# Performance work log

Hardware: AMD Instinct MI355X
Metric: run time of the kernel (lower is better)

The kernel has to match this reference:

```python
import jax, jax.numpy as jnp
import numpy as np

N_NODES = 100000

def setup_inputs() -> dict:
    key = jax.random.key(0)
    k1, k2, k3 = jax.random.split(key, 3)
    x = jax.random.normal(k1, (N_NODES, 128), dtype=jnp.float32)
    edge_index = jax.random.randint(k2, (2, 1600000), 0, N_NODES, dtype=jnp.int64)
    W = jax.random.normal(k3, (128, 128), dtype=jnp.float32) * 0.05  # Linear weight [out, in]
    b = jnp.zeros((128,), dtype=jnp.float32)
    return {"x": x, "edge_index": edge_index, "W": W, "b": b}

def reference(x, edge_index, W, b):
    # GCNConv (PyG defaults): normalize=True, add_self_loops=True, bias=True.
    N = x.shape[0]
    # 1) linear transform (no bias inside)
    h = x @ W.T  # [N, H]
    # 2) add self loops
    loops = jnp.arange(N, dtype=edge_index.dtype)
    src = jnp.concatenate([edge_index[0], loops])  # source (x_j)
    dst = jnp.concatenate([edge_index[1], loops])  # target (aggregation)
    # 3) symmetric degree normalization: deg over target nodes with unit weights
    deg = jax.ops.segment_sum(jnp.ones_like(dst, dtype=h.dtype), dst, num_segments=N)
    dinv = jnp.where(deg > 0, jax.lax.rsqrt(deg), 0.0)
    norm = dinv[src] * dinv[dst]  # [E+N]
    # 4) gather-scale-scatter aggregation
    msgs = h[src] * norm[:, None]  # [E+N, H]
    out = jax.ops.segment_sum(msgs, dst, num_segments=N)
    # 5) bias
    return out + b
```

## Files before the change

### kernel.cpp

```cpp
#include <hip/hip_runtime.h>

#define H 128
#define NREG 8
#define KE 16
#define TILE (256 * KE)
#define LINB 512
#define B2T 2048
#define SCAP 3072
#define RCAP 220160

typedef __attribute__((ext_vector_type(8))) short short8_t;
typedef __attribute__((ext_vector_type(4))) float float4_t;

__device__ __forceinline__ ushort f2bf(float f) {
  uint u = __float_as_uint(f);
  u += 0x7fff + ((u >> 16) & 1);
  return (ushort)(u >> 16);
}
__device__ __forceinline__ float bflo(uint v) { return __uint_as_float(v << 16); }
__device__ __forceinline__ float bfhi(uint v) { return __uint_as_float(v & 0xffff0000u); }

__global__ __launch_bounds__(256) void k_linbin(const float* __restrict__ x, const float* __restrict__ W,
                                                ushort* __restrict__ hs,
                                                const int* __restrict__ src, const int* __restrict__ dst,
                                                int* gcur, int* __restrict__ breg,
                                                int N, int E, int npr) {
  __shared__ int cntw[4][NREG];
  __shared__ int basew[4][NREG];
  __shared__ int lpre8[NREG + 1];
  __shared__ int gbase8[NREG];
  __shared__ int staged[TILE];
  const int tid = threadIdx.x;

  if (blockIdx.x < LINB) {
    const int lane = tid & 63;
    const int wid  = tid >> 6;
    const int rg   = wid >> 1;
    const int cg   = wid & 1;
    const int q    = lane >> 4;
    const int lm   = lane & 15;

    short8_t bfr[4][4];
    #pragma unroll
    for (int kk = 0; kk < 4; ++kk) {
      #pragma unroll
      for (int nf = 0; nf < 4; ++nf) {
        const float* wp = W + (cg * 64 + nf * 16 + lm) * 128 + kk * 32 + q * 8;
        float4_t w0 = *(const float4_t*)wp;
        float4_t w1 = *(const float4_t*)(wp + 4);
        union { short8_t s; ushort u[8]; } t;
        t.u[0] = f2bf(w0.x); t.u[1] = f2bf(w0.y); t.u[2] = f2bf(w0.z); t.u[3] = f2bf(w0.w);
        t.u[4] = f2bf(w1.x); t.u[5] = f2bf(w1.y); t.u[6] = f2bf(w1.z); t.u[7] = f2bf(w1.w);
        bfr[kk][nf] = t.s;
      }
    }

    const int ntiles = (N + 31) / 32;
    for (int tile = blockIdx.x; tile < ntiles; tile += LINB) {
      const int n0 = tile * 32;
      const int arow = n0 + rg * 16 + lm;
      const int arow_c = (arow < N) ? arow : (N - 1);
      const float* xp = x + (long)arow_c * H + q * 8;
      short8_t afr[4];
      #pragma unroll
      for (int kk = 0; kk < 4; ++kk) {
        float4_t x0 = *(const float4_t*)(xp + kk * 32);
        float4_t x1 = *(const float4_t*)(xp + kk * 32 + 4);
        union { short8_t s; ushort u[8]; } t;
        t.u[0] = f2bf(x0.x); t.u[1] = f2bf(x0.y); t.u[2] = f2bf(x0.z); t.u[3] = f2bf(x0.w);
        t.u[4] = f2bf(x1.x); t.u[5] = f2bf(x1.y); t.u[6] = f2bf(x1.z); t.u[7] = f2bf(x1.w);
        afr[kk] = t.s;
      }

      float4_t acc[4];
      #pragma unroll
      for (int nf = 0; nf < 4; ++nf) acc[nf] = (float4_t){0.f, 0.f, 0.f, 0.f};
      #pragma unroll
      for (int kk = 0; kk < 4; ++kk) {
        #pragma unroll
        for (int nf = 0; nf < 4; ++nf)
          acc[nf] = __builtin_amdgcn_mfma_f32_16x16x32_bf16(bfr[kk][nf], afr[kk], acc[nf], 0, 0, 0);
      }

      if (arow < N) {
        ushort* hrow = hs + (size_t)arow * H + cg * 64 + q * 4;
        #pragma unroll
        for (int nf = 0; nf < 4; ++nf) {
          uint2 o;
          o.x = (uint)f2bf(acc[nf][0]) | ((uint)f2bf(acc[nf][1]) << 16);
          o.y = (uint)f2bf(acc[nf][2]) | ((uint)f2bf(acc[nf][3]) << 16);
          *(uint2*)(hrow + nf * 16) = o;
        }
      }
    }
  } else {
    const int bb = blockIdx.x - LINB;
    const int wv = tid >> 6;
    if (tid < 32) cntw[tid >> 3][tid & 7] = 0;
    __syncthreads();
    const int base = bb * TILE;
    int pk[KE], r[KE], off[KE];
    #pragma unroll
    for (int k = 0; k < KE; ++k) {
      const int e = base + k * 256 + tid;
      if (e < E) {
        const int s = src[e], d = dst[e];
        r[k] = (int)((unsigned)d / (unsigned)npr);
        pk[k] = (s << 14) | (d - r[k] * npr);
        off[k] = atomicAdd(&cntw[wv][r[k]], 1);
      } else r[k] = -1;
    }
    __syncthreads();
    if (tid == 0) {
      int acc = 0;
      #pragma unroll
      for (int j = 0; j < NREG; ++j) {
        lpre8[j] = acc;
        #pragma unroll
        for (int w2 = 0; w2 < 4; ++w2) { basew[w2][j] = acc; acc += cntw[w2][j]; }
      }
      lpre8[NREG] = acc;
    }
    __syncthreads();
    if (tid < NREG) gbase8[tid] = atomicAdd(&gcur[tid], lpre8[tid + 1] - lpre8[tid]);
    #pragma unroll
    for (int k = 0; k < KE; ++k)
      if (r[k] >= 0) staged[basew[wv][r[k]] + off[k]] = pk[k];
    __syncthreads();
    const int tot = lpre8[NREG];
    for (int i = tid; i < tot; i += 256) {
      int reg = 0;
      #pragma unroll
      for (int j = 1; j < NREG; ++j) reg += (i >= lpre8[j]);
      const int p = gbase8[reg] + (i - lpre8[reg]);
      if (p < RCAP) breg[reg * RCAP + p] = staged[i];
    }
  }
}

__global__ __launch_bounds__(256) void k_bin2(const int* __restrict__ breg, const int* __restrict__ gcur,
                                              int* cur2, int* __restrict__ bsub, int nsub) {
  __shared__ int cnt[128], lcur[128], lpre[128], gb[128];
  __shared__ int staged[B2T];
  const int tid = threadIdx.x;
  const int r = blockIdx.x & 7;
  const int t0 = (blockIdx.x >> 3) * B2T;
  const int total = min(gcur[r], RCAP);
  if (t0 >= total) return;
  const int cntT = min(B2T, total - t0);
  for (int i = tid; i < 128; i += 256) { cnt[i] = 0; lcur[i] = 0; }
  __syncthreads();
  const int* bp = breg + (size_t)r * RCAP + t0;
  for (int i = tid; i < cntT; i += 256) atomicAdd(&cnt[(bp[i] >> 7) & 127], 1);
  __syncthreads();
  if (tid < 128) lpre[tid] = cnt[tid];
  __syncthreads();
  for (int off = 1; off < 128; off <<= 1) {
    int v = 0;
    if (tid < 128 && tid >= off) v = lpre[tid - off];
    __syncthreads();
    if (tid < 128) lpre[tid] += v;
    __syncthreads();
  }
  if (tid < 128) {
    lpre[tid] -= cnt[tid];
    const int c = cnt[tid];
    gb[tid] = c ? atomicAdd(&cur2[r * nsub + tid], c) : 0;
  }
  __syncthreads();
  for (int i = tid; i < cntT; i += 256) {
    const int v = bp[i];
    const int sub = (v >> 7) & 127;
    const int pos = lpre[sub] + atomicAdd(&lcur[sub], 1);
    staged[pos] = (sub << 24) | ((v >> 14) << 7) | (v & 127);
  }
  __syncthreads();
  for (int i = tid; i < cntT; i += 256) {
    const int v = staged[i];
    const int sub = (int)((unsigned)v >> 24);
    const int pos = gb[sub] + (i - lpre[sub]);
    if (pos < SCAP) bsub[((size_t)(r * nsub + sub)) * SCAP + pos] = v & 0xFFFFFF;
  }
}

__global__ __launch_bounds__(256) void k_fill3(const int* __restrict__ bsub, const int* __restrict__ cur2,
                                               float* __restrict__ dinv, uint4* __restrict__ rowinfo,
                                               int* __restrict__ csr, int N, int npr, int nsub) {
  __shared__ int cnt[128], pre[128], lcur[128];
  __shared__ int stage[SCAP], sorted[SCAP];
  const int tid = threadIdx.x;
  const int r = blockIdx.x & 7;
  const int sub = blockIdx.x >> 3;
  const int sid = r * nsub + sub;
  const int gn0 = r * npr + sub * 128;
  int nodes = npr - sub * 128; if (nodes > 128) nodes = 128;
  if (N - gn0 < nodes) nodes = N - gn0;
  if (nodes <= 0) return;
  if (tid < 128) cnt[tid] = 0;
  __syncthreads();

  const int slotbase = sid * SCAP;
  const int cc = min(cur2[sid], SCAP);
  const int* bp = bsub + (size_t)slotbase;
  for (int i = tid; i < cc; i += 256) {
    const int v = bp[i];
    stage[i] = v;
    atomicAdd(&cnt[v & 127], 1);
  }
  __syncthreads();

  if (tid < 128) pre[tid] = cnt[tid];
  __syncthreads();
  for (int off = 1; off < 128; off <<= 1) {
    int v = 0;
    if (tid < 128 && tid >= off) v = pre[tid - off];
    __syncthreads();
    if (tid < 128) pre[tid] += v;
    __syncthreads();
  }
  if (tid < 128) pre[tid] -= cnt[tid];
  __syncthreads();

  if (tid < nodes) {
    const int c = cnt[tid];
    const float dv = rsqrtf((float)(1 + c));
    dinv[gn0 + tid] = dv;
    rowinfo[gn0 + tid] = make_uint4((uint)(slotbase + pre[tid]), (uint)c, __float_as_uint(dv), 0u);
    lcur[tid] = pre[tid];
  }
  __syncthreads();

  for (int i = tid; i < cc; i += 256) {
    const int v = stage[i];
    const int p = atomicAdd(&lcur[v & 127], 1);
    sorted[p] = (int)((unsigned)v >> 7);
  }
  __syncthreads();
  for (int i = tid; i < cc; i += 256) csr[slotbase + i] = sorted[i];
}

#define ACCS(q, ds) { a0 = fmaf(bflo((q).x), ds, a0); a1 = fmaf(bfhi((q).x), ds, a1); \
                      a2 = fmaf(bflo((q).y), ds, a2); a3 = fmaf(bfhi((q).y), ds, a3); \
                      a4 = fmaf(bflo((q).z), ds, a4); a5 = fmaf(bfhi((q).z), ds, a5); \
                      a6 = fmaf(bflo((q).w), ds, a6); a7 = fmaf(bfhi((q).w), ds, a7); }
__global__ __launch_bounds__(256) void k_agg(const ushort* __restrict__ hs, const float* __restrict__ dinv,
                                             const uint4* __restrict__ rowinfo, const int* __restrict__ csr,
                                             const float* __restrict__ bias, float* __restrict__ out,
                                             int N, int npr) {
  const int r = blockIdx.x & 7;
  const int ln = (blockIdx.x >> 3) * 16 + (threadIdx.x >> 4);
  if (ln >= npr) return;
  const int d = r * npr + ln;
  if (d >= N) return;
  const int j = threadIdx.x & 15;
  const uint4* hp = (const uint4*)hs;

  const uint4 info = rowinfo[d];
  int i = (int)info.x;
  int cnt = (int)info.y;
  const float dd = __uint_as_float(info.z);

  const uint4 qs = hp[(size_t)d * 16 + j];
  float a0 = bflo(qs.x) * dd, a1 = bfhi(qs.x) * dd, a2 = bflo(qs.y) * dd, a3 = bfhi(qs.y) * dd;
  float a4 = bflo(qs.z) * dd, a5 = bfhi(qs.z) * dd, a6 = bflo(qs.w) * dd, a7 = bfhi(qs.w) * dd;

  for (; cnt >= 8; cnt -= 8, i += 8) {
    const int s0 = csr[i],     s1 = csr[i + 1], s2 = csr[i + 2], s3 = csr[i + 3];
    const int s4 = csr[i + 4], s5 = csr[i + 5], s6 = csr[i + 6], s7 = csr[i + 7];
    const float d0 = dinv[s0], d1 = dinv[s1], d2 = dinv[s2], d3 = dinv[s3];
    const float d4 = dinv[s4], d5 = dinv[s5], d6 = dinv[s6], d7 = dinv[s7];
    const uint4 qA = hp[(size_t)s0 * 16 + j];
    const uint4 qB = hp[(size_t)s1 * 16 + j];
    const uint4 qC = hp[(size_t)s2 * 16 + j];
    const uint4 qD = hp[(size_t)s3 * 16 + j];
    const uint4 qE = hp[(size_t)s4 * 16 + j];
    const uint4 qF = hp[(size_t)s5 * 16 + j];
    const uint4 qG = hp[(size_t)s6 * 16 + j];
    const uint4 qH = hp[(size_t)s7 * 16 + j];
    ACCS(qA, d0) ACCS(qB, d1) ACCS(qC, d2) ACCS(qD, d3)
    ACCS(qE, d4) ACCS(qF, d5) ACCS(qG, d6) ACCS(qH, d7)
  }
  if (cnt >= 4) {
    const int s0 = csr[i], s1 = csr[i + 1], s2 = csr[i + 2], s3 = csr[i + 3];
    const float d0 = dinv[s0], d1 = dinv[s1], d2 = dinv[s2], d3 = dinv[s3];
    const uint4 qA = hp[(size_t)s0 * 16 + j];
    const uint4 qB = hp[(size_t)s1 * 16 + j];
    const uint4 qC = hp[(size_t)s2 * 16 + j];
    const uint4 qD = hp[(size_t)s3 * 16 + j];
    ACCS(qA, d0) ACCS(qB, d1) ACCS(qC, d2) ACCS(qD, d3)
    cnt -= 4; i += 4;
  }
  for (; cnt > 0; --cnt, ++i) {
    const int s = csr[i];
    const float ds = dinv[s];
    const uint4 q = hp[(size_t)s * 16 + j];
    ACCS(q, ds)
  }

  const float4_t b0 = *(const float4_t*)(bias + j * 8);
  const float4_t b1 = *(const float4_t*)(bias + j * 8 + 4);
  float4_t o0, o1;
  o0.x = a0 * dd + b0.x; o0.y = a1 * dd + b0.y; o0.z = a2 * dd + b0.z; o0.w = a3 * dd + b0.w;
  o1.x = a4 * dd + b1.x; o1.y = a5 * dd + b1.y; o1.z = a6 * dd + b1.z; o1.w = a7 * dd + b1.w;
  __builtin_nontemporal_store(o0, (float4_t*)(out + (size_t)d * H + j * 8));
  __builtin_nontemporal_store(o1, (float4_t*)(out + (size_t)d * H + j * 8 + 4));
}

extern "C" void kernel_launch(void* const* d_in, const int* in_sizes, int n_in,
                              void* d_out, int out_size, void* d_ws, size_t ws_size,
                              hipStream_t stream) {
  const float* x = (const float*)d_in[0];
  const int*   edge = (const int*)d_in[1];
  const float* W = (const float*)d_in[2];
  const float* b = (const float*)d_in[3];
  float* out = (float*)d_out;

  const int N = in_sizes[0] / H;
  const int E = in_sizes[1] / 2;
  const int* src = edge;
  const int* dst = edge + E;
  const int npr  = (N + NREG - 1) / NREG;
  const int nsub = (npr + 127) / 128;
  const int nsubt = NREG * nsub;

  char* w = (char*)d_ws;
  ushort* hs     = (ushort*)w;  w += (size_t)N * H * 2;
  float*  dinv   = (float*)w;   w += (size_t)N * 4;
  int*    gcur   = (int*)w;     w += (size_t)NREG * 4;
  int*    cur2   = (int*)w;     w += (size_t)nsubt * 4;
  uint4*  rowinfo= (uint4*)w;   w += (size_t)N * 16;
  int*    csr    = (int*)w;     w += (size_t)nsubt * SCAP * 4;
  int*    breg   = (int*)w;     w += (size_t)NREG * RCAP * 4;
  int*    bsub   = (int*)w;     w += (size_t)nsubt * SCAP * 4;
  (void)ws_size;

  (void)hipMemsetAsync(gcur, 0, (size_t)(NREG + nsubt) * 4, stream);

  const int nbin = (E + TILE - 1) / TILE;
  const int bpr2 = (RCAP + B2T - 1) / B2T;
  k_linbin<<<LINB + nbin, 256, 0, stream>>>(x, W, hs, src, dst, gcur, breg, N, E, npr);
  k_bin2<<<8 * bpr2, 256, 0, stream>>>(breg, gcur, cur2, bsub, nsub);
  k_fill3<<<nsubt, 256, 0, stream>>>(bsub, cur2, dinv, rowinfo, csr, N, npr, nsub);
  k_agg<<<8 * ((npr + 15) / 16), 256, 0, stream>>>(hs, dinv, rowinfo, csr, b, out, N, npr);
}
```

Before: 127.3 us.

## Split linear transform across bin2 and fill3 kernels to overlap with binning

The dense x@W^T MFMA work moves out of the first binning kernel and is split in two halves. One half is co-scheduled as extra blocks in the second-level binning kernel, the other in the CSR fill kernel. The first-level bin kernel now runs alone. The aim is to balance compute-heavy linear tiles against memory/atomic-heavy binning stages so each launch uses the GPU more evenly. The cost is more blocks per launch and fewer linear blocks per tile range, which may change occupancy, since fill3 uses large shared memory.

```diff
diff --git a/kernel.cpp b/kernel.cpp
--- a/kernel.cpp
+++ b/kernel.cpp
@@ -4,8 +4,9 @@
 #define NREG 8
 #define KE 16
 #define TILE (256 * KE)
-#define LINB 512
 #define B2T 2048
+#define NB2 (8 * ((RCAP + B2T - 1) / B2T))
+#define LINB2 768
 #define SCAP 3072
 #define RCAP 220160
 
@@ -20,129 +21,133 @@
 __device__ __forceinline__ float bflo(uint v) { return __uint_as_float(v << 16); }
 __device__ __forceinline__ float bfhi(uint v) { return __uint_as_float(v & 0xffff0000u); }
 
-__global__ __launch_bounds__(256) void k_linbin(const float* __restrict__ x, const float* __restrict__ W,
-                                                ushort* __restrict__ hs,
-                                                const int* __restrict__ src, const int* __restrict__ dst,
-                                                int* gcur, int* __restrict__ breg,
-                                                int N, int E, int npr) {
+__device__ __forceinline__ void linear_range(const float* __restrict__ x, const float* __restrict__ W,
+                                             ushort* __restrict__ hs, int N,
+                                             int tile0, int tend, int tid) {
+  const int lane = tid & 63;
+  const int wid  = tid >> 6;
+  const int rg   = wid >> 1;
+  const int cg   = wid & 1;
+  const int q    = lane >> 4;
+  const int lm   = lane & 15;
+
+  short8_t bfr[4][4];
+  #pragma unroll
+  for (int kk = 0; kk < 4; ++kk) {
+    #pragma unroll
+    for (int nf = 0; nf < 4; ++nf) {
+      const float* wp = W + (cg * 64 + nf * 16 + lm) * 128 + kk * 32 + q * 8;
+      float4_t w0 = *(const float4_t*)wp;
+      float4_t w1 = *(const float4_t*)(wp + 4);
+      union { short8_t s; ushort u[8]; } t;
+      t.u[0] = f2bf(w0.x); t.u[1] = f2bf(w0.y); t.u[2] = f2bf(w0.z); t.u[3] = f2bf(w0.w);
+      t.u[4] = f2bf(w1.x); t.u[5] = f2bf(w1.y); t.u[6] = f2bf(w1.z); t.u[7] = f2bf(w1.w);
+      bfr[kk][nf] = t.s;
+    }
+  }
+
+  for (int tile = tile0; tile < tend; tile += LINB2) {
+    const int n0 = tile * 32;
+    const int arow = n0 + rg * 16 + lm;
+    const int arow_c = (arow < N) ? arow : (N - 1);
+    const float* xp = x + (long)arow_c * H + q * 8;
+    short8_t afr[4];
+    #pragma unroll
+    for (int kk = 0; kk < 4; ++kk) {
+      float4_t x0 = *(const float4_t*)(xp + kk * 32);
+      float4_t x1 = *(const float4_t*)(xp + kk * 32 + 4);
+      union { short8_t s; ushort u[8]; } t;
+      t.u[0] = f2bf(x0.x); t.u[1] = f2bf(x0.y); t.u[2] = f2bf(x0.z); t.u[3] = f2bf(x0.w);
+      t.u[4] = f2bf(x1.x); t.u[5] = f2bf(x1.y); t.u[6] = f2bf(x1.z); t.u[7] = f2bf(x1.w);
+      afr[kk] = t.s;
+    }
+
+    float4_t acc[4];
+    #pragma unroll
+    for (int nf = 0; nf < 4; ++nf) acc[nf] = (float4_t){0.f, 0.f, 0.f, 0.f};
+    #pragma unroll
+    for (int kk = 0; kk < 4; ++kk) {
+      #pragma unroll
+      for (int nf = 0; nf < 4; ++nf)
+        acc[nf] = __builtin_amdgcn_mfma_f32_16x16x32_bf16(bfr[kk][nf], afr[kk], acc[nf], 0, 0, 0);
+    }
+
+    if (arow < N) {
+      ushort* hrow = hs + (size_t)arow * H + cg * 64 + q * 4;
+      #pragma unroll
+      for (int nf = 0; nf < 4; ++nf) {
+        uint2 o;
+        o.x = (uint)f2bf(acc[nf][0]) | ((uint)f2bf(acc[nf][1]) << 16);
+        o.y = (uint)f2bf(acc[nf][2]) | ((uint)f2bf(acc[nf][3]) << 16);
+        *(uint2*)(hrow + nf * 16) = o;
+      }
+    }
+  }
+}
+
+__global__ __launch_bounds__(256) void k_bin(const int* __restrict__ src, const int* __restrict__ dst,
+                                             int* gcur, int* __restrict__ breg, int E, int npr) {
   __shared__ int cntw[4][NREG];
   __shared__ int basew[4][NREG];
   __shared__ int lpre8[NREG + 1];
   __shared__ int gbase8[NREG];
   __shared__ int staged[TILE];
   const int tid = threadIdx.x;
-
-  if (blockIdx.x < LINB) {
-    const int lane = tid & 63;
-    const int wid  = tid >> 6;
-    const int rg   = wid >> 1;
-    const int cg   = wid & 1;
-    const int q    = lane >> 4;
-    const int lm   = lane & 15;
-
-    short8_t bfr[4][4];
-    #pragma unroll
-    for (int kk = 0; kk < 4; ++kk) {
+  const int wv = tid >> 6;
+  if (tid < 32) cntw[tid >> 3][tid & 7] = 0;
+  __syncthreads();
+  const int base = blockIdx.x * TILE;
+  int pk[KE], r[KE], off[KE];
+  #pragma unroll
+  for (int k = 0; k < KE; ++k) {
+    const int e = base + k * 256 + tid;
+    if (e < E) {
+      const int s = src[e], d = dst[e];
+      r[k] = (int)((unsigned)d / (unsigned)npr);
+      pk[k] = (s << 14) | (d - r[k] * npr);
+      off[k] = atomicAdd(&cntw[wv][r[k]], 1);
+    } else r[k] = -1;
+  }
+  __syncthreads();
+  if (tid == 0) {
+    int acc = 0;
+    #pragma unroll
+    for (int j = 0; j < NREG; ++j) {
+      lpre8[j] = acc;
       #pragma unroll
-      for (int nf = 0; nf < 4; ++nf) {
-        const float* wp = W + (cg * 64 + nf * 16 + lm) * 128 + kk * 32 + q * 8;
-        float4_t w0 = *(const float4_t*)wp;
-        float4_t w1 = *(const float4_t*)(wp + 4);
-        union { short8_t s; ushort u[8]; } t;
-        t.u[0] = f2bf(w0.x); t.u[1] = f2bf(w0.y); t.u[2] = f2bf(w0.z); t.u[3] = f2bf(w0.w);
-        t.u[4] = f2bf(w1.x); t.u[5] = f2bf(w1.y); t.u[6] = f2bf(w1.z); t.u[7] = f2bf(w1.w);
-        bfr[kk][nf] = t.s;
-      }
-    }
-
-    const int ntiles = (N + 31) / 32;
-    for (int tile = blockIdx.x; tile < ntiles; tile += LINB) {
-      const int n0 = tile * 32;
-      const int arow = n0 + rg * 16 + lm;
-      const int arow_c = (arow < N) ? arow : (N - 1);
-      const float* xp = x + (long)arow_c * H + q * 8;
-      short8_t afr[4];
-      #pragma unroll
-      for (int kk = 0; kk < 4; ++kk) {
-        float4_t x0 = *(const float4_t*)(xp + kk * 32);
-        float4_t x1 = *(const float4_t*)(xp + kk * 32 + 4);
-        union { short8_t s; ushort u[8]; } t;
-        t.u[0] = f2bf(x0.x); t.u[1] = f2bf(x0.y); t.u[2] = f2bf(x0.z); t.u[3] = f2bf(x0.w);
-        t.u[4] = f2bf(x1.x); t.u[5] = f2bf(x1.y); t.u[6] = f2bf(x1.z); t.u[7] = f2bf(x1.w);
-        afr[kk] = t.s;
-      }
-
-      float4_t acc[4];
-      #pragma unroll
-      for (int nf = 0; nf < 4; ++nf) acc[nf] = (float4_t){0.f, 0.f, 0.f, 0.f};
-      #pragma unroll
-      for (int kk = 0; kk < 4; ++kk) {
-        #pragma unroll
-        for (int nf = 0; nf < 4; ++nf)
-          acc[nf] = __builtin_amdgcn_mfma_f32_16x16x32_bf16(bfr[kk][nf], afr[kk], acc[nf], 0, 0, 0);
-      }
-
-      if (arow < N) {
-        ushort* hrow = hs + (size_t)arow * H + cg * 64 + q * 4;
-        #pragma unroll
-        for (int nf = 0; nf < 4; ++nf) {
-          uint2 o;
-          o.x = (uint)f2bf(acc[nf][0]) | ((uint)f2bf(acc[nf][1]) << 16);
-          o.y = (uint)f2bf(acc[nf][2]) | ((uint)f2bf(acc[nf][3]) << 16);
-          *(uint2*)(hrow + nf * 16) = o;
-        }
-      }
-    }
-  } else {
-    const int bb = blockIdx.x - LINB;
-    const int wv = tid >> 6;
-    if (tid < 32) cntw[tid >> 3][tid & 7] = 0;
-    __syncthreads();
-    const int base = bb * TILE;
-    int pk[KE], r[KE], off[KE];
-    #pragma unroll
-    for (int k = 0; k < KE; ++k) {
-      const int e = base + k * 256 + tid;
-      if (e < E) {
-        const int s = src[e], d = dst[e];
-        r[k] = (int)((unsigned)d / (unsigned)npr);
-        pk[k] = (s << 14) | (d - r[k] * npr);
-        off[k] = atomicAdd(&cntw[wv][r[k]], 1);
-      } else r[k] = -1;
-    }
-    __syncthreads();
-    if (tid == 0) {
-      int acc = 0;
-      #pragma unroll
-      for (int j = 0; j < NREG; ++j) {
-        lpre8[j] = acc;
-        #pragma unroll
-        for (int w2 = 0; w2 < 4; ++w2) { basew[w2][j] = acc; acc += cntw[w2][j]; }
-      }
-      lpre8[NREG] = acc;
-    }
-    __syncthreads();
-    if (tid < NREG) gbase8[tid] = atomicAdd(&gcur[tid], lpre8[tid + 1] - lpre8[tid]);
-    #pragma unroll
-    for (int k = 0; k < KE; ++k)
-      if (r[k] >= 0) staged[basew[wv][r[k]] + off[k]] = pk[k];
-    __syncthreads();
-    const int tot = lpre8[NREG];
-    for (int i = tid; i < tot; i += 256) {
-      int reg = 0;
-      #pragma unroll
-      for (int j = 1; j < NREG; ++j) reg += (i >= lpre8[j]);
-      const int p = gbase8[reg] + (i - lpre8[reg]);
-      if (p < RCAP) breg[reg * RCAP + p] = staged[i];
-    }
-  }
-}
-
-__global__ __launch_bounds__(256) void k_bin2(const int* __restrict__ breg, const int* __restrict__ gcur,
-                                              int* cur2, int* __restrict__ bsub, int nsub) {
+      for (int w2 = 0; w2 < 4; ++w2) { basew[w2][j] = acc; acc += cntw[w2][j]; }
+    }
+    lpre8[NREG] = acc;
+  }
+  __syncthreads();
+  if (tid < NREG) gbase8[tid] = atomicAdd(&gcur[tid], lpre8[tid + 1] - lpre8[tid]);
+  #pragma unroll
+  for (int k = 0; k < KE; ++k)
+    if (r[k] >= 0) staged[basew[wv][r[k]] + off[k]] = pk[k];
+  __syncthreads();
+  const int tot = lpre8[NREG];
+  for (int i = tid; i < tot; i += 256) {
+    int reg = 0;
+    #pragma unroll
+    for (int j = 1; j < NREG; ++j) reg += (i >= lpre8[j]);
+    const int p = gbase8[reg] + (i - lpre8[reg]);
+    if (p < RCAP) breg[reg * RCAP + p] = staged[i];
+  }
+}
+
+__global__ __launch_bounds__(256) void k_bin2lin(const int* __restrict__ breg, const int* __restrict__ gcur,
+                                                 int* cur2, int* __restrict__ bsub, int nsub,
+                                                 const float* __restrict__ x, const float* __restrict__ W,
+                                                 ushort* __restrict__ hs, int N, int tsplit) {
   __shared__ int cnt[128], lcur[128], lpre[128], gb[128];
   __shared__ int staged[B2T];
   const int tid = threadIdx.x;
+
+  if (blockIdx.x >= NB2) {
+    linear_range(x, W, hs, N, blockIdx.x - NB2, tsplit, tid);
+    return;
+  }
+
   const int r = blockIdx.x & 7;
   const int t0 = (blockIdx.x >> 3) * B2T;
   const int total = min(gcur[r], RCAP);
@@ -183,12 +188,20 @@
   }
 }
 
-__global__ __launch_bounds__(256) void k_fill3(const int* __restrict__ bsub, const int* __restrict__ cur2,
-                                               float* __restrict__ dinv, uint4* __restrict__ rowinfo,
-                                               int* __restrict__ csr, int N, int npr, int nsub) {
+__global__ __launch_bounds__(256) void k_fill3lin(const int* __restrict__ bsub, const int* __restrict__ cur2,
+                                                  float* __restrict__ dinv, uint4* __restrict__ rowinfo,
+                                                  int* __restrict__ csr, int N, int npr, int nsub, int nsort,
+                                                  const float* __restrict__ x, const float* __restrict__ W,
+                                                  ushort* __restrict__ hs, int tsplit, int ntiles) {
   __shared__ int cnt[128], pre[128], lcur[128];
   __shared__ int stage[SCAP], sorted[SCAP];
   const int tid = threadIdx.x;
+
+  if (blockIdx.x >= nsort) {
+    linear_range(x, W, hs, N, tsplit + (blockIdx.x - nsort), ntiles, tid);
+    return;
+  }
+
   const int r = blockIdx.x & 7;
   const int sub = blockIdx.x >> 3;
   const int sid = r * nsub + sub;
@@ -322,6 +335,8 @@
   const int npr  = (N + NREG - 1) / NREG;
   const int nsub = (npr + 127) / 128;
   const int nsubt = NREG * nsub;
+  const int ntiles = (N + 31) / 32;
+  const int tsplit = (ntiles + 1) / 2;
 
   char* w = (char*)d_ws;
   ushort* hs     = (ushort*)w;  w += (size_t)N * H * 2;
@@ -337,9 +352,9 @@
   (void)hipMemsetAsync(gcur, 0, (size_t)(NREG + nsubt) * 4, stream);
 
   const int nbin = (E + TILE - 1) / TILE;
-  const int bpr2 = (RCAP + B2T - 1) / B2T;
-  k_linbin<<<LINB + nbin, 256, 0, stream>>>(x, W, hs, src, dst, gcur, breg, N, E, npr);
-  k_bin2<<<8 * bpr2, 256, 0, stream>>>(breg, gcur, cur2, bsub, nsub);
-  k_fill3<<<nsubt, 256, 0, stream>>>(bsub, cur2, dinv, rowinfo, csr, N, npr, nsub);
+  k_bin<<<nbin, 256, 0, stream>>>(src, dst, gcur, breg, E, npr);
+  k_bin2lin<<<NB2 + LINB2, 256, 0, stream>>>(breg, gcur, cur2, bsub, nsub, x, W, hs, N, tsplit);
+  k_fill3lin<<<nsubt + LINB2, 256, 0, stream>>>(bsub, cur2, dinv, rowinfo, csr, N, npr, nsub, nsubt,
+                                                x, W, hs, tsplit, ntiles);
   k_agg<<<8 * ((npr + 15) / 16), 256, 0, stream>>>(hs, dinv, rowinfo, csr, b, out, N, npr);
 }
```

Result: slower. 150.4 us (+18.2%).

## Bin edges directly into 128-node sub-buckets, dropping the two-level region pass

Applied to the files above, without the earlier changes.

Replaces the two-pass binning (8 regions, then 128-node sub-buckets in a separate kernel) with a single pass that buckets each edge tile straight into about 782 sub-buckets. It uses a block-wide scan in shared memory and per-bucket global atomics. The intermediate region buffer and one kernel launch go away, along with a full read and write of all edges. In exchange, each binning block does many more global atomics and scattered small writes, and shared-memory use grows, which may lower occupancy of the combined linear/binning kernel.

```diff
diff --git a/kernel.cpp b/kernel.cpp
--- a/kernel.cpp
+++ b/kernel.cpp
@@ -1,13 +1,11 @@
 #include <hip/hip_runtime.h>
 
 #define H 128
-#define NREG 8
 #define KE 16
 #define TILE (256 * KE)
 #define LINB 512
-#define B2T 2048
+#define NSUBMAX 784
 #define SCAP 3072
-#define RCAP 220160
 
 typedef __attribute__((ext_vector_type(8))) short short8_t;
 typedef __attribute__((ext_vector_type(4))) float float4_t;
@@ -23,13 +21,14 @@
 __global__ __launch_bounds__(256) void k_linbin(const float* __restrict__ x, const float* __restrict__ W,
                                                 ushort* __restrict__ hs,
                                                 const int* __restrict__ src, const int* __restrict__ dst,
-                                                int* gcur, int* __restrict__ breg,
-                                                int N, int E, int npr) {
-  __shared__ int cntw[4][NREG];
-  __shared__ int basew[4][NREG];
-  __shared__ int lpre8[NREG + 1];
-  __shared__ int gbase8[NREG];
+                                                int* cur2, int* __restrict__ bsub,
+                                                int N, int E, int nsubt) {
+  __shared__ int cnt[NSUBMAX];
+  __shared__ int lbase[NSUBMAX];
+  __shared__ int gbase[NSUBMAX];
+  __shared__ int ls[256];
   __shared__ int staged[TILE];
+  __shared__ ushort sstage[TILE];
   const int tid = threadIdx.x;
 
   if (blockIdx.x < LINB) {
@@ -95,106 +94,76 @@
     }
   } else {
     const int bb = blockIdx.x - LINB;
-    const int wv = tid >> 6;
-    if (tid < 32) cntw[tid >> 3][tid & 7] = 0;
-    __syncthreads();
+    for (int i = tid; i < NSUBMAX; i += 256) cnt[i] = 0;
+    __syncthreads();
+
     const int base = bb * TILE;
-    int pk[KE], r[KE], off[KE];
+    int pk[KE], off[KE];
+    short sd[KE];
     #pragma unroll
     for (int k = 0; k < KE; ++k) {
       const int e = base + k * 256 + tid;
       if (e < E) {
         const int s = src[e], d = dst[e];
-        r[k] = (int)((unsigned)d / (unsigned)npr);
-        pk[k] = (s << 14) | (d - r[k] * npr);
-        off[k] = atomicAdd(&cntw[wv][r[k]], 1);
-      } else r[k] = -1;
-    }
-    __syncthreads();
-    if (tid == 0) {
-      int acc = 0;
-      #pragma unroll
-      for (int j = 0; j < NREG; ++j) {
-        lpre8[j] = acc;
-        #pragma unroll
-        for (int w2 = 0; w2 < 4; ++w2) { basew[w2][j] = acc; acc += cntw[w2][j]; }
-      }
-      lpre8[NREG] = acc;
-    }
-    __syncthreads();
-    if (tid < NREG) gbase8[tid] = atomicAdd(&gcur[tid], lpre8[tid + 1] - lpre8[tid]);
+        const int sid = d >> 7;
+        pk[k] = (s << 7) | (d & 127);
+        sd[k] = (short)sid;
+        off[k] = atomicAdd(&cnt[sid], 1);
+      } else sd[k] = -1;
+    }
+    __syncthreads();
+
+    int tsum = 0;
+    if (tid < NSUBMAX / 4) {
+      #pragma unroll
+      for (int j = 0; j < 4; ++j) tsum += cnt[4 * tid + j];
+    }
+    ls[tid] = tsum;
+    __syncthreads();
+    for (int o = 1; o < 256; o <<= 1) {
+      int v = (tid >= o) ? ls[tid - o] : 0;
+      __syncthreads();
+      ls[tid] += v;
+      __syncthreads();
+    }
+    const int tot = ls[255];
+    if (tid < NSUBMAX / 4) {
+      int b = ls[tid] - tsum;
+      #pragma unroll
+      for (int j = 0; j < 4; ++j) { lbase[4 * tid + j] = b; b += cnt[4 * tid + j]; }
+    }
+    __syncthreads();
+    for (int i = tid; i < nsubt; i += 256) {
+      const int c = cnt[i];
+      gbase[i] = c ? atomicAdd(&cur2[i], c) : 0;
+    }
+    __syncthreads();
     #pragma unroll
-    for (int k = 0; k < KE; ++k)
-      if (r[k] >= 0) staged[basew[wv][r[k]] + off[k]] = pk[k];
-    __syncthreads();
-    const int tot = lpre8[NREG];
+    for (int k = 0; k < KE; ++k) {
+      if (sd[k] >= 0) {
+        const int p = lbase[sd[k]] + off[k];
+        staged[p] = pk[k];
+        sstage[p] = (ushort)sd[k];
+      }
+    }
+    __syncthreads();
     for (int i = tid; i < tot; i += 256) {
-      int reg = 0;
-      #pragma unroll
-      for (int j = 1; j < NREG; ++j) reg += (i >= lpre8[j]);
-      const int p = gbase8[reg] + (i - lpre8[reg]);
-      if (p < RCAP) breg[reg * RCAP + p] = staged[i];
-    }
-  }
-}
-
-__global__ __launch_bounds__(256) void k_bin2(const int* __restrict__ breg, const int* __restrict__ gcur,
-                                              int* cur2, int* __restrict__ bsub, int nsub) {
-  __shared__ int cnt[128], lcur[128], lpre[128], gb[128];
-  __shared__ int staged[B2T];
-  const int tid = threadIdx.x;
-  const int r = blockIdx.x & 7;
-  const int t0 = (blockIdx.x >> 3) * B2T;
-  const int total = min(gcur[r], RCAP);
-  if (t0 >= total) return;
-  const int cntT = min(B2T, total - t0);
-  for (int i = tid; i < 128; i += 256) { cnt[i] = 0; lcur[i] = 0; }
-  __syncthreads();
-  const int* bp = breg + (size_t)r * RCAP + t0;
-  for (int i = tid; i < cntT; i += 256) atomicAdd(&cnt[(bp[i] >> 7) & 127], 1);
-  __syncthreads();
-  if (tid < 128) lpre[tid] = cnt[tid];
-  __syncthreads();
-  for (int off = 1; off < 128; off <<= 1) {
-    int v = 0;
-    if (tid < 128 && tid >= off) v = lpre[tid - off];
-    __syncthreads();
-    if (tid < 128) lpre[tid] += v;
-    __syncthreads();
-  }
-  if (tid < 128) {
-    lpre[tid] -= cnt[tid];
-    const int c = cnt[tid];
-    gb[tid] = c ? atomicAdd(&cur2[r * nsub + tid], c) : 0;
-  }
-  __syncthreads();
-  for (int i = tid; i < cntT; i += 256) {
-    const int v = bp[i];
-    const int sub = (v >> 7) & 127;
-    const int pos = lpre[sub] + atomicAdd(&lcur[sub], 1);
-    staged[pos] = (sub << 24) | ((v >> 14) << 7) | (v & 127);
-  }
-  __syncthreads();
-  for (int i = tid; i < cntT; i += 256) {
-    const int v = staged[i];
-    const int sub = (int)((unsigned)v >> 24);
-    const int pos = gb[sub] + (i - lpre[sub]);
-    if (pos < SCAP) bsub[((size_t)(r * nsub + sub)) * SCAP + pos] = v & 0xFFFFFF;
+      const int sid = sstage[i];
+      const int p = gbase[sid] + (i - lbase[sid]);
+      if (p < SCAP) bsub[(size_t)sid * SCAP + p] = staged[i];
+    }
   }
 }
 
 __global__ __launch_bounds__(256) void k_fill3(const int* __restrict__ bsub, const int* __restrict__ cur2,
                                                float* __restrict__ dinv, uint4* __restrict__ rowinfo,
-                                               int* __restrict__ csr, int N, int npr, int nsub) {
+                                               int* __restrict__ csr, int N) {
   __shared__ int cnt[128], pre[128], lcur[128];
   __shared__ int stage[SCAP], sorted[SCAP];
   const int tid = threadIdx.x;
-  const int r = blockIdx.x & 7;
-  const int sub = blockIdx.x >> 3;
-  const int sid = r * nsub + sub;
-  const int gn0 = r * npr + sub * 128;
-  int nodes = npr - sub * 128; if (nodes > 128) nodes = 128;
-  if (N - gn0 < nodes) nodes = N - gn0;
+  const int sid = blockIdx.x;
+  const int gn0 = sid * 128;
+  int nodes = N - gn0; if (nodes > 128) nodes = 128;
   if (nodes <= 0) return;
   if (tid < 128) cnt[tid] = 0;
   __syncthreads();
@@ -245,12 +214,8 @@
                       a6 = fmaf(bflo((q).w), ds, a6); a7 = fmaf(bfhi((q).w), ds, a7); }
 __global__ __launch_bounds__(256) void k_agg(const ushort* __restrict__ hs, const float* __restrict__ dinv,
                                              const uint4* __restrict__ rowinfo, const int* __restrict__ csr,
-                                             const float* __restrict__ bias, float* __restrict__ out,
-                                             int N, int npr) {
-  const int r = blockIdx.x & 7;
-  const int ln = (blockIdx.x >> 3) * 16 + (threadIdx.x >> 4);
-  if (ln >= npr) return;
-  const int d = r * npr + ln;
+                                             const float* __restrict__ bias, float* __restrict__ out, int N) {
+  const int d = blockIdx.x * 16 + (threadIdx.x >> 4);
   if (d >= N) return;
   const int j = threadIdx.x & 15;
   const uint4* hp = (const uint4*)hs;
@@ -319,27 +284,21 @@
   const int E = in_sizes[1] / 2;
   const int* src = edge;
   const int* dst = edge + E;
-  const int npr  = (N + NREG - 1) / NREG;
-  const int nsub = (npr + 127) / 128;
-  const int nsubt = NREG * nsub;
+  const int nsubt = (N + 127) / 128;
 
   char* w = (char*)d_ws;
   ushort* hs     = (ushort*)w;  w += (size_t)N * H * 2;
   float*  dinv   = (float*)w;   w += (size_t)N * 4;
-  int*    gcur   = (int*)w;     w += (size_t)NREG * 4;
-  int*    cur2   = (int*)w;     w += (size_t)nsubt * 4;
+  int*    cur2   = (int*)w;     w += (size_t)NSUBMAX * 4;
   uint4*  rowinfo= (uint4*)w;   w += (size_t)N * 16;
   int*    csr    = (int*)w;     w += (size_t)nsubt * SCAP * 4;
-  int*    breg   = (int*)w;     w += (size_t)NREG * RCAP * 4;
   int*    bsub   = (int*)w;     w += (size_t)nsubt * SCAP * 4;
   (void)ws_size;
 
-  (void)hipMemsetAsync(gcur, 0, (size_t)(NREG + nsubt) * 4, stream);
+  (void)hipMemsetAsync(cur2, 0, (size_t)NSUBMAX * 4, stream);
 
   const int nbin = (E + TILE - 1) / TILE;
-  const int bpr2 = (RCAP + B2T - 1) / B2T;
-  k_linbin<<<LINB + nbin, 256, 0, stream>>>(x, W, hs, src, dst, gcur, breg, N, E, npr);
-  k_bin2<<<8 * bpr2, 256, 0, stream>>>(breg, gcur, cur2, bsub, nsub);
-  k_fill3<<<nsubt, 256, 0, stream>>>(bsub, cur2, dinv, rowinfo, csr, N, npr, nsub);
-  k_agg<<<8 * ((npr + 15) / 16), 256, 0, stream>>>(hs, dinv, rowinfo, csr, b, out, N, npr);
-}
+  k_linbin<<<LINB + nbin, 256, 0, stream>>>(x, W, hs, src, dst, cur2, bsub, N, E, nsubt);
+  k_fill3<<<nsubt, 256, 0, stream>>>(bsub, cur2, dinv, rowinfo, csr, N);
+  k_agg<<<(N + 15) / 16, 256, 0, stream>>>(hs, dinv, rowinfo, csr, b, out, N);
+}
```

Result: faster. 122.3 us, median of 2 (-3.9%).
